# Kernel optimization log

Hardware: AMD Instinct MI355X
Metric: run time of the kernel (lower is better)

## Reference

```python
import jax, jax.numpy as jnp
import numpy as np

B, T, H, K = 4, 4096, 2048, 4
FREQ_BINS = H // 2  # int(hidden_size * freq_ratio) with freq_ratio=0.5


def setup_inputs() -> dict:
    key = jax.random.key(0)
    k1, k2 = jax.random.split(key, 2)
    x = jax.random.normal(k1, (B, T, H), dtype=jnp.float32)
    # kernel_weights = ones + 0.02*randn, shape (n_kernels, freq_bins)
    kernel_weights = 1.0 + 0.02 * jax.random.normal(k2, (K, FREQ_BINS), dtype=jnp.float32)
    thresholds = jnp.full((K,), 0.1, dtype=jnp.float32)
    # blend_proj: Linear(n_kernels, 1, bias=False), weight (1, K) init to 1/K
    blend_w = jnp.full((1, K), 1.0 / K, dtype=jnp.float32)
    return {"x": x, "kernel_weights": kernel_weights, "thresholds": thresholds, "blend_w": blend_w}


def reference(x, kernel_weights, thresholds, blend_w):
    # energy per token: L2 norm over hidden dim -> (B, T)
    energy = jnp.linalg.norm(x, axis=-1)
    # threshold-gated routing: (B, T, K) binary gate (non-differentiable)
    gate = (energy[..., None] > jnp.abs(thresholds)[None, None, :]).astype(jnp.float32)
    # rfft over hidden dim, keep real part of first freq_bins bins
    fb = kernel_weights.shape[1]
    x_fft_real = jnp.fft.rfft(x.astype(jnp.float32), axis=-1).real[..., :fb]  # (B, T, fb)
    # per-kernel spectral projection
    scaled = jnp.einsum('btf,kf->btk', x_fft_real, kernel_weights)  # (B, T, K)
    activated = scaled * gate
    # blend to scalar map + tanh -> (B, T, 1)
    mod = jnp.tanh(jnp.einsum('btk,ok->bto', activated, blend_w))
    return mod.astype(x.dtype)
```

## Files before the change

### kernel.cpp

```cpp
#include <hip/hip_runtime.h>
#include <math.h>

#define HDIM 2048
#define FB   1024
#define NK   4
#define NTOK 16384

__global__ __launch_bounds__(256) void build_eff(const float* __restrict__ w,
                                                 float* __restrict__ e) {
    int gid = blockIdx.x * 256 + threadIdx.x;
    int oid = gid >> 4;
    int sub = gid & 15;
    int k = oid >> 11;
    int n = oid & 2047;
    const float* wk = w + k * FB;

    const float c = 6.283185307179586f / 2048.0f;
    int step = (n << 4) & 2047;
    int p = (n * sub) & 2047;
    float acc = 0.0f;
#pragma unroll 8
    for (int j = 0; j < 64; ++j) {
        int f = (j << 4) + sub;
        acc = fmaf(wk[f], cosf((float)p * c), acc);
        p = (p + step) & 2047;
    }
    acc += __shfl_xor(acc, 1);
    acc += __shfl_xor(acc, 2);
    acc += __shfl_xor(acc, 4);
    acc += __shfl_xor(acc, 8);
    if (sub == 0) e[oid] = acc;
}

__global__ __launch_bounds__(256) void spectral_main(
    const float* __restrict__ x,
    const float* __restrict__ e,
    const float* __restrict__ thr,
    const float* __restrict__ blend,
    float* __restrict__ out) {
    __shared__ float4 els[NK * HDIM / 4];

    int tid = threadIdx.x;
    const float4* eg = (const float4*)e;
#pragma unroll
    for (int i = 0; i < 8; ++i) els[i * 256 + tid] = eg[i * 256 + tid];
    __syncthreads();

    float th0 = fabsf(thr[0]), th1 = fabsf(thr[1]);
    float th2 = fabsf(thr[2]), th3 = fabsf(thr[3]);
    float b0 = blend[0], b1 = blend[1], b2 = blend[2], b3 = blend[3];

    int wave = tid >> 6;
    int lane = tid & 63;
    int tokbase = blockIdx.x * 16 + wave * 4;

    for (int i = 0; i < 4; ++i) {
        int tok = tokbase + i;
        const float4* xr = (const float4*)(x + (size_t)tok * HDIM);
        float en = 0.0f, a0 = 0.0f, a1 = 0.0f, a2 = 0.0f, a3 = 0.0f;
#pragma unroll
        for (int cच = 0; cच < 8; ++cच) {
            int idx = cच * 64 + lane;
            float4 xv = xr[idx];
            float4 e0 = els[0 * 512 + idx];
            float4 e1 = els[1 * 512 + idx];
            float4 e2 = els[2 * 512 + idx];
            float4 e3 = els[3 * 512 + idx];
            en = fmaf(xv.x, xv.x, fmaf(xv.y, xv.y, fmaf(xv.z, xv.z, fmaf(xv.w, xv.w, en))));
            a0 = fmaf(xv.x, e0.x, fmaf(xv.y, e0.y, fmaf(xv.z, e0.z, fmaf(xv.w, e0.w, a0))));
            a1 = fmaf(xv.x, e1.x, fmaf(xv.y, e1.y, fmaf(xv.z, e1.z, fmaf(xv.w, e1.w, a1))));
            a2 = fmaf(xv.x, e2.x, fmaf(xv.y, e2.y, fmaf(xv.z, e2.z, fmaf(xv.w, e2.w, a2))));
            a3 = fmaf(xv.x, e3.x, fmaf(xv.y, e3.y, fmaf(xv.z, e3.z, fmaf(xv.w, e3.w, a3))));
        }
#pragma unroll
        for (int s = 1; s < 64; s <<= 1) {
            en += __shfl_xor(en, s);
            a0 += __shfl_xor(a0, s);
            a1 += __shfl_xor(a1, s);
            a2 += __shfl_xor(a2, s);
            a3 += __shfl_xor(a3, s);
        }
        if (lane == 0) {
            float energy = sqrtf(en);
            float z = 0.0f;
            if (energy > th0) z = fmaf(b0, a0, z);
            if (energy > th1) z = fmaf(b1, a1, z);
            if (energy > th2) z = fmaf(b2, a2, z);
            if (energy > th3) z = fmaf(b3, a3, z);
            out[tok] = tanhf(z);
        }
    }
}

extern "C" void kernel_launch(void* const* d_in, const int* in_sizes, int n_in,
                              void* d_out, int out_size, void* d_ws, size_t ws_size,
                              hipStream_t stream) {
    const float* x     = (const float*)d_in[0];
    const float* w     = (const float*)d_in[1];
    const float* thr   = (const float*)d_in[2];
    const float* blend = (const float*)d_in[3];
    float* out = (float*)d_out;
    float* e   = (float*)d_ws;

    build_eff<<<512, 256, 0, stream>>>(w, e);
    spectral_main<<<NTOK / 16, 256, 0, stream>>>(x, e, thr, blend, out);
}
```

Baseline: 35.08 us.

## Process four tokens per wave jointly and use hardware cosine in weight prep

The main kernel now loads each wave's four tokens at the same time, so each LDS read of the effective weights is reused across four tokens, and the memory loads for the tokens overlap. The shuffle reductions are interleaved across tokens and the four outputs are written as one float4 store. The weight-building kernel swaps cosf for the native amdgcn cos builtin, which takes its input in revolutions, cutting the cost of the trig calls at some loss of accuracy. Register use goes up (20 accumulators plus 4 float4 loads), which may reduce occupancy.

```diff
diff --git a/kernel.cpp b/kernel.cpp
--- a/kernel.cpp
+++ b/kernel.cpp
@@ -15,14 +15,14 @@
     int n = oid & 2047;
     const float* wk = w + k * FB;
 
-    const float c = 6.283185307179586f / 2048.0f;
+    const float inv = 1.0f / 2048.0f;
     int step = (n << 4) & 2047;
     int p = (n * sub) & 2047;
     float acc = 0.0f;
 #pragma unroll 8
     for (int j = 0; j < 64; ++j) {
         int f = (j << 4) + sub;
-        acc = fmaf(wk[f], cosf((float)p * c), acc);
+        acc = fmaf(wk[f], __builtin_amdgcn_cosf((float)p * inv), acc);
         p = (p + step) & 2047;
     }
     acc += __shfl_xor(acc, 1);
@@ -30,6 +30,16 @@
     acc += __shfl_xor(acc, 4);
     acc += __shfl_xor(acc, 8);
     if (sub == 0) e[oid] = acc;
+}
+
+__device__ __forceinline__ float finish_tok(float en, const float* a,
+                                            const float* th, const float* bl) {
+    float energy = sqrtf(en);
+    float z = 0.0f;
+#pragma unroll
+    for (int k = 0; k < NK; ++k)
+        if (energy > th[k]) z = fmaf(bl[k], a[k], z);
+    return tanhf(z);
 }
 
 __global__ __launch_bounds__(256) void spectral_main(
@@ -46,49 +56,57 @@
     for (int i = 0; i < 8; ++i) els[i * 256 + tid] = eg[i * 256 + tid];
     __syncthreads();
 
-    float th0 = fabsf(thr[0]), th1 = fabsf(thr[1]);
-    float th2 = fabsf(thr[2]), th3 = fabsf(thr[3]);
-    float b0 = blend[0], b1 = blend[1], b2 = blend[2], b3 = blend[3];
+    float th[NK], bl[NK];
+#pragma unroll
+    for (int k = 0; k < NK; ++k) { th[k] = fabsf(thr[k]); bl[k] = blend[k]; }
 
     int wave = tid >> 6;
     int lane = tid & 63;
-    int tokbase = blockIdx.x * 16 + wave * 4;
+    int tok0 = blockIdx.x * 16 + wave * 4;
+    const float4* xr = (const float4*)x + (size_t)tok0 * (HDIM / 4);
 
-    for (int i = 0; i < 4; ++i) {
-        int tok = tokbase + i;
-        const float4* xr = (const float4*)(x + (size_t)tok * HDIM);
-        float en = 0.0f, a0 = 0.0f, a1 = 0.0f, a2 = 0.0f, a3 = 0.0f;
+    float en[4] = {0.f, 0.f, 0.f, 0.f};
+    float ac[4][NK] = {};
+
 #pragma unroll
-        for (int cच = 0; cच < 8; ++cच) {
-            int idx = cच * 64 + lane;
-            float4 xv = xr[idx];
-            float4 e0 = els[0 * 512 + idx];
-            float4 e1 = els[1 * 512 + idx];
-            float4 e2 = els[2 * 512 + idx];
-            float4 e3 = els[3 * 512 + idx];
-            en = fmaf(xv.x, xv.x, fmaf(xv.y, xv.y, fmaf(xv.z, xv.z, fmaf(xv.w, xv.w, en))));
-            a0 = fmaf(xv.x, e0.x, fmaf(xv.y, e0.y, fmaf(xv.z, e0.z, fmaf(xv.w, e0.w, a0))));
-            a1 = fmaf(xv.x, e1.x, fmaf(xv.y, e1.y, fmaf(xv.z, e1.z, fmaf(xv.w, e1.w, a1))));
-            a2 = fmaf(xv.x, e2.x, fmaf(xv.y, e2.y, fmaf(xv.z, e2.z, fmaf(xv.w, e2.w, a2))));
-            a3 = fmaf(xv.x, e3.x, fmaf(xv.y, e3.y, fmaf(xv.z, e3.z, fmaf(xv.w, e3.w, a3))));
+    for (int c = 0; c < 8; ++c) {
+        int idx = c * 64 + lane;
+        float4 ev[NK];
+#pragma unroll
+        for (int k = 0; k < NK; ++k) ev[k] = els[k * 512 + idx];
+        float4 xv[4];
+#pragma unroll
+        for (int t = 0; t < 4; ++t) xv[t] = xr[t * 512 + idx];
+#pragma unroll
+        for (int t = 0; t < 4; ++t) {
+            float4 v = xv[t];
+            en[t] = fmaf(v.x, v.x, fmaf(v.y, v.y, fmaf(v.z, v.z, fmaf(v.w, v.w, en[t]))));
+#pragma unroll
+            for (int k = 0; k < NK; ++k) {
+                float4 w4 = ev[k];
+                ac[t][k] = fmaf(v.x, w4.x, fmaf(v.y, w4.y,
+                           fmaf(v.z, w4.z, fmaf(v.w, w4.w, ac[t][k]))));
+            }
         }
+    }
+
 #pragma unroll
-        for (int s = 1; s < 64; s <<= 1) {
-            en += __shfl_xor(en, s);
-            a0 += __shfl_xor(a0, s);
-            a1 += __shfl_xor(a1, s);
-            a2 += __shfl_xor(a2, s);
-            a3 += __shfl_xor(a3, s);
+    for (int s = 1; s < 64; s <<= 1) {
+#pragma unroll
+        for (int t = 0; t < 4; ++t) {
+            en[t] += __shfl_xor(en[t], s);
+#pragma unroll
+            for (int k = 0; k < NK; ++k) ac[t][k] += __shfl_xor(ac[t][k], s);
         }
-        if (lane == 0) {
-            float energy = sqrtf(en);
-            float z = 0.0f;
-            if (energy > th0) z = fmaf(b0, a0, z);
-            if (energy > th1) z = fmaf(b1, a1, z);
-            if (energy > th2) z = fmaf(b2, a2, z);
-            if (energy > th3) z = fmaf(b3, a3, z);
-            out[tok] = tanhf(z);
-        }
+    }
+
+    if (lane == 0) {
+        float4 o;
+        o.x = finish_tok(en[0], ac[0], th, bl);
+        o.y = finish_tok(en[1], ac[1], th, bl);
+        o.z = finish_tok(en[2], ac[2], th, bl);
+        o.w = finish_tok(en[3], ac[3], th, bl);
+        *(float4*)(out + tok0) = o;
     }
 }
 
```

Measured after the change: 34.70 us. Within noise of the previous version (-1.1%).
